# Optimization experiments

Hardware: AMD Instinct MI355X
Metric: run time of the kernel (lower is better)

Reference implementation:

```python
import jax, jax.numpy as jnp
import numpy as np

ENCODER_DIM = 2048
DECODER_DIM = 512
ATTENTION_DIM = 512
BATCH = 512
NUM_PIXELS = 196


def setup_inputs() -> dict:
    key = jax.random.key(0)
    k = jax.random.split(key, 8)
    s_e = 1.0 / np.sqrt(ENCODER_DIM)
    s_d = 1.0 / np.sqrt(DECODER_DIM)
    s_a = 1.0 / np.sqrt(ATTENTION_DIM)
    return {
        "encoder_out": jax.random.normal(k[0], (BATCH, NUM_PIXELS, ENCODER_DIM), jnp.float32),
        "decoder_hidden": jax.random.normal(k[1], (BATCH, DECODER_DIM), jnp.float32),
        "W_enc": jax.random.uniform(k[2], (ENCODER_DIM, ATTENTION_DIM), jnp.float32, -s_e, s_e),
        "b_enc": jax.random.uniform(k[3], (ATTENTION_DIM,), jnp.float32, -s_e, s_e),
        "W_dec": jax.random.uniform(k[4], (DECODER_DIM, ATTENTION_DIM), jnp.float32, -s_d, s_d),
        "b_dec": jax.random.uniform(k[5], (ATTENTION_DIM,), jnp.float32, -s_d, s_d),
        "W_full": jax.random.uniform(k[6], (ATTENTION_DIM,), jnp.float32, -s_a, s_a),
        "b_full": jax.random.uniform(k[7], (), jnp.float32, -s_a, s_a),
    }


def reference(encoder_out, decoder_hidden, W_enc, b_enc, W_dec, b_dec, W_full, b_full):
    # att1: [B, P, A], att2: [B, A]
    att1 = jnp.einsum('bpe,ea->bpa', encoder_out, W_enc) + b_enc
    att2 = decoder_hidden @ W_dec + b_dec
    # scores: [B, P]
    scores = jnp.einsum('bpa,a->bp', jnp.tanh(att1 + att2[:, None, :]), W_full) + b_full
    alpha = jax.nn.softmax(scores, axis=1)
    context = jnp.einsum('bpe,bp->be', encoder_out, alpha)
    return context, alpha
```

## Files before the change

### kernel.cpp

```cpp
#include <hip/hip_runtime.h>
#include <hip/hip_bf16.h>
#include <stdint.h>

#define BATCH 512
#define PIX   196
#define EDIM  2048
#define DDIM  512
#define ADIM  512
#define MROWS (BATCH*PIX)

#define BM 256
#define BN 256
#define BK 32
#define NT (EDIM/BK)

typedef __attribute__((ext_vector_type(8))) short bf16x8;
typedef __attribute__((ext_vector_type(8))) float f32x8;
typedef __attribute__((ext_vector_type(8))) __bf16 bf16v8;
typedef __attribute__((ext_vector_type(4))) float f32x4;

#define GLL16(g, lptr) __builtin_amdgcn_global_load_lds( \
    (const __attribute__((address_space(1))) void*)(g),  \
    (__attribute__((address_space(3))) void*)(lptr), 16, 0, 0)

static __device__ __forceinline__ unsigned short f2bf(float f) {
  union { float f; uint32_t u; } v; v.f = f;
  uint32_t u = v.u;
  return (unsigned short)((u + 0x7FFFu + ((u >> 16) & 1u)) >> 16);
}

static __device__ __forceinline__ bf16x8 cvt8(float4 a, float4 b) {
  f32x8 v = {a.x, a.y, a.z, a.w, b.x, b.y, b.z, b.w};
  bf16v8 c = __builtin_convertvector(v, bf16v8);
  bf16x8 r;
  __builtin_memcpy(&r, &c, 16);
  return r;
}

__global__ void k_transpose_wenc(const float* __restrict__ W,
                                 unsigned short* __restrict__ Bt) {
  __shared__ float tile[32][33];
  const int kt = blockIdx.x;
  const int nt = blockIdx.y;
  const int tx = threadIdx.x, ty = threadIdx.y;
#pragma unroll
  for (int j = 0; j < 4; j++)
    tile[ty + 8*j][tx] = W[(size_t)(kt*32 + ty + 8*j)*ADIM + nt*32 + tx];
  __syncthreads();
#pragma unroll
  for (int j = 0; j < 4; j++)
    Bt[(size_t)(nt*32 + ty + 8*j)*EDIM + kt*32 + tx] = f2bf(tile[tx][ty + 8*j]);
}

__global__ void k_att2(const float* __restrict__ H, const float* __restrict__ Wd,
                       const float* __restrict__ bd, float* __restrict__ att2) {
  __shared__ float h[DDIM];
  const int b = blockIdx.x;
  const int t = threadIdx.x;
  h[t]       = H[(size_t)b*DDIM + t];
  h[t + 256] = H[(size_t)b*DDIM + t + 256];
  __syncthreads();
  float a0 = 0.f, a1 = 0.f;
#pragma unroll 8
  for (int k = 0; k < DDIM; k++) {
    const float hv = h[k];
    a0 += hv * Wd[(size_t)k*ADIM + t];
    a1 += hv * Wd[(size_t)k*ADIM + t + 256];
  }
  att2[(size_t)b*ADIM + t]       = a0 + bd[t];
  att2[(size_t)b*ADIM + t + 256] = a1 + bd[t + 256];
}

__global__ __launch_bounds__(512) void k_gemm_scores(
    const float* __restrict__ enc,
    const unsigned short* __restrict__ Bt,
    const float* __restrict__ b_enc,
    const float* __restrict__ att2,
    const float* __restrict__ W_full,
    float* __restrict__ scores)
{
  __shared__ __align__(16) char ldsbuf[3*49152];
  __shared__ float sc[BM];
  char* ldsA = ldsbuf;
  char* ldsB = ldsbuf + 98304;

  const int t   = threadIdx.x;
  const int l   = t & 63;
  const int wid = t >> 6;
  const int wr  = wid >> 2;
  const int wc  = wid & 3;

  const int orig = blockIdx.x;
  const int tile = (orig & 7) * 98 + (orig >> 3);
  const int bm0 = (tile >> 1) * BM;
  const int bn0 = (tile & 1) * BN;

  if (t < BM) sc[t] = 0.f;

  const float* srcA[4];
#pragma unroll
  for (int j = 0; j < 4; j++) {
    const int idx = j*512 + t;
    const int row = idx >> 3, c = idx & 7;
    srcA[j] = enc + (size_t)(bm0 + row) * EDIM + (c ^ (row & 7)) * 4;
  }
  const unsigned short* srcB[2];
#pragma unroll
  for (int j = 0; j < 2; j++) {
    const int idx = j*512 + t;
    const int row = idx >> 2, c = idx & 3;
    srcB[j] = Bt + (size_t)(bn0 + row) * EDIM + (c ^ (row & 3)) * 8;
  }
  const int dstb = wid * 1024;

  const int l15 = l & 15, hi = l >> 4;
  const int sw7 = l15 & 7, sw3 = l15 & 3;
  const int addrA0 = (wr*128 + l15)*128 + (((2*hi)    ) ^ sw7)*16;
  const int addrA1 = (wr*128 + l15)*128 + (((2*hi) + 1) ^ sw7)*16;
  const int addrB  = (wc*64  + l15)*64  + (hi ^ sw3)*16;

  bf16x8 af[4], bfr[4];
  f32x4 acc[8][4] = {};

#define A_GLL(WB, KT) do {                                       \
    _Pragma("unroll")                                            \
    for (int j = 0; j < 4; j++)                                  \
      GLL16(srcA[j] + (size_t)(KT)*BK,                           \
            ldsA + (WB)*32768 + j*8192 + dstb);                  \
  } while (0)

#define B_GLL(WB, KT) do {                                       \
    _Pragma("unroll")                                            \
    for (int j = 0; j < 2; j++)                                  \
      GLL16(srcB[j] + (size_t)(KT)*BK,                           \
            ldsB + (WB)*16384 + j*8192 + dstb);                  \
  } while (0)

#define DSREAD_A(BUF, MOFF) do {                                 \
    _Pragma("unroll")                                            \
    for (int mi = 0; mi < 4; mi++) {                             \
      const float4 fa = *(const float4*)(ldsA + (BUF)*32768 + (mi+(MOFF))*2048 + addrA0); \
      const float4 fb = *(const float4*)(ldsA + (BUF)*32768 + (mi+(MOFF))*2048 + addrA1); \
      af[mi] = cvt8(fa, fb);                                     \
    }                                                            \
  } while (0)

#define DSREAD_B(BUF) do {                                       \
    _Pragma("unroll")                                            \
    for (int ni = 0; ni < 4; ni++)                               \
      bfr[ni] = *(const bf16x8*)(ldsB + (BUF)*16384 + ni*1024 + addrB); \
  } while (0)

#define BARLG()                                                  \
    __builtin_amdgcn_s_barrier();                                \
    asm volatile("s_waitcnt lgkmcnt(0)" ::: "memory");           \
    __builtin_amdgcn_sched_barrier(0);                           \
    __builtin_amdgcn_s_setprio(1)

#define ENDBAR()                                                 \
    __builtin_amdgcn_s_setprio(0);                               \
    __builtin_amdgcn_s_barrier()

#define MF16(MOFF) do {                                          \
    _Pragma("unroll")                                            \
    for (int mi = 0; mi < 4; mi++)                               \
      _Pragma("unroll")                                          \
      for (int ni = 0; ni < 4; ni++)                             \
        acc[mi+(MOFF)][ni] = __builtin_amdgcn_mfma_f32_16x16x32_bf16( \
            af[mi], bfr[ni], acc[mi+(MOFF)][ni], 0, 0, 0);       \
  } while (0)

#define TILE(T, BUF, WBUF, DO_STAGE, WVM) do {                   \
                                                         \
    if (DO_STAGE) A_GLL(WBUF, (T)+2);                            \
    DSREAD_B(BUF); DSREAD_A(BUF, 0);                             \
    BARLG(); MF16(0); ENDBAR();                                  \
                                                         \
    if (DO_STAGE) B_GLL(WBUF, (T)+2);                            \
    DSREAD_A(BUF, 4);                                            \
    BARLG(); MF16(4);                                            \
    if ((WVM) == 6)      asm volatile("s_waitcnt vmcnt(6)" ::: "memory"); \
    else if ((WVM) == 0) asm volatile("s_waitcnt vmcnt(0)" ::: "memory"); \
    ENDBAR();                                                    \
  } while (0)

  A_GLL(0, 0); B_GLL(0, 0);
  A_GLL(1, 1); B_GLL(1, 1);
  asm volatile("s_waitcnt vmcnt(6)" ::: "memory");
  __builtin_amdgcn_s_barrier();

  for (int kb = 0; kb < 60; kb += 3) {
    TILE(kb,     0, 2, true, 6);
    TILE(kb + 1, 1, 0, true, 6);
    TILE(kb + 2, 2, 1, true, 6);
  }
  TILE(60, 0, 2, true, 6);
  TILE(61, 1, 0, true, 6);
  TILE(62, 2, 2, false, 0);
  DSREAD_B(0); DSREAD_A(0, 0); MF16(0);
  DSREAD_A(0, 4); MF16(4);

  float be[4], wf[4];
  int colv[4];
#pragma unroll
  for (int ni = 0; ni < 4; ni++) {
    colv[ni] = bn0 + wc*64 + ni*16 + l15;
    be[ni] = b_enc[colv[ni]];
    wf[ni] = W_full[colv[ni]];
  }
#pragma unroll
  for (int mi = 0; mi < 8; mi++) {
#pragma unroll
    for (int e = 0; e < 4; e++) {
      const int row_l = wr*128 + mi*16 + hi*4 + e;
      const unsigned gr = (unsigned)(bm0 + row_l);
      const unsigned b  = gr / 196u;
      float s = 0.f;
#pragma unroll
      for (int ni = 0; ni < 4; ni++) {
        const float v = acc[mi][ni][e] + be[ni] + att2[(size_t)b*ADIM + colv[ni]];
        s += tanhf(v) * wf[ni];
      }
      s += __shfl_xor(s, 1); s += __shfl_xor(s, 2);
      s += __shfl_xor(s, 4); s += __shfl_xor(s, 8);
      if (l15 == 0) atomicAdd(&sc[row_l], s);
    }
  }
  __syncthreads();
  if (t < BM) atomicAdd(&scores[bm0 + t], sc[t]);
}

__global__ void k_softmax(float* __restrict__ sa) {
  __shared__ float red[256];
  const int b = blockIdx.x, t = threadIdx.x;
  const float v = (t < PIX) ? sa[(size_t)b*PIX + t] : -1e30f;
  red[t] = v; __syncthreads();
  for (int s2 = 128; s2 > 0; s2 >>= 1) {
    if (t < s2) red[t] = fmaxf(red[t], red[t + s2]);
    __syncthreads();
  }
  const float m = red[0]; __syncthreads();
  const float e = (t < PIX) ? __expf(v - m) : 0.f;
  red[t] = e; __syncthreads();
  for (int s2 = 128; s2 > 0; s2 >>= 1) {
    if (t < s2) red[t] += red[t + s2];
    __syncthreads();
  }
  const float inv = 1.f / red[0];
  if (t < PIX) sa[(size_t)b*PIX + t] = e * inv;
}

__global__ __launch_bounds__(512) void k_context(
    const float* __restrict__ enc, const float* __restrict__ alpha,
    float* __restrict__ ctx) {
  __shared__ float al[PIX];
  const int b = blockIdx.x, t = threadIdx.x;
  if (t < PIX) al[t] = alpha[(size_t)b*PIX + t];
  __syncthreads();
  const float4* e4 = (const float4*)(enc + (size_t)b * PIX * EDIM);
  float4 acc = {0.f, 0.f, 0.f, 0.f};
#pragma unroll 4
  for (int p = 0; p < PIX; p++) {
    const float4 v = e4[(size_t)p * (EDIM/4) + t];
    const float a = al[p];
    acc.x += v.x * a; acc.y += v.y * a; acc.z += v.z * a; acc.w += v.w * a;
  }
  ((float4*)(ctx + (size_t)b * EDIM))[t] = acc;
}

extern "C" void kernel_launch(void* const* d_in, const int* in_sizes, int n_in,
                              void* d_out, int out_size, void* d_ws, size_t ws_size,
                              hipStream_t stream) {
  (void)in_sizes; (void)n_in; (void)out_size; (void)ws_size;
  const float* enc   = (const float*)d_in[0];
  const float* hid   = (const float*)d_in[1];
  const float* Wenc  = (const float*)d_in[2];
  const float* benc  = (const float*)d_in[3];
  const float* Wdec  = (const float*)d_in[4];
  const float* bdec  = (const float*)d_in[5];
  const float* Wfull = (const float*)d_in[6];

  unsigned short* Bt = (unsigned short*)d_ws;
  float* att2 = (float*)((char*)d_ws + (size_t)ADIM * EDIM * 2);
  float* ctx   = (float*)d_out;
  float* alpha = (float*)d_out + (size_t)BATCH * EDIM;

  hipMemsetAsync(alpha, 0, (size_t)MROWS * sizeof(float), stream);
  k_transpose_wenc<<<dim3(64, 16), dim3(32, 8), 0, stream>>>(Wenc, Bt);
  k_att2<<<BATCH, 256, 0, stream>>>(hid, Wdec, bdec, att2);
  k_gemm_scores<<<784, 512, 0, stream>>>(enc, Bt, benc, att2, Wfull, alpha);
  k_softmax<<<BATCH, 256, 0, stream>>>(alpha);
  k_context<<<BATCH, 512, 0, stream>>>(enc, alpha, ctx);
}
```

Before: 667.3 us.

## Shrink GEMM tile to 256x128, convert A to bf16 in registers before LDS store

The fused score GEMM now uses 256-thread blocks with a 256x128 output tile and two blocks per CU, launching twice as many blocks. The A operand is loaded from global into registers, converted to bf16 once, and written to LDS in bf16. Previously it was staged as fp32 via global_load_lds and converted on every LDS read. LDS use drops sharply and the pipeline goes from three buffers to two, with a register-prefetched A tile. The trade-off is that the encoder tile is reread four times across N-tiles instead of twice, raising global traffic on the dominant fp32 input.

```diff
diff --git a/kernel.cpp b/kernel.cpp
--- a/kernel.cpp
+++ b/kernel.cpp
@@ -10,7 +10,7 @@
 #define MROWS (BATCH*PIX)
 
 #define BM 256
-#define BN 256
+#define BN 128
 #define BK 32
 #define NT (EDIM/BK)
 
@@ -71,7 +71,7 @@
   att2[(size_t)b*ADIM + t + 256] = a1 + bd[t + 256];
 }
 
-__global__ __launch_bounds__(512) void k_gemm_scores(
+__global__ __launch_bounds__(256, 2) void k_gemm_scores(
     const float* __restrict__ enc,
     const unsigned short* __restrict__ Bt,
     const float* __restrict__ b_enc,
@@ -79,87 +79,76 @@
     const float* __restrict__ W_full,
     float* __restrict__ scores)
 {
-  __shared__ __align__(16) char ldsbuf[3*49152];
+  __shared__ __align__(16) char ldsA[2*16384];
+  __shared__ __align__(16) char ldsB[2*8192];
   __shared__ float sc[BM];
-  char* ldsA = ldsbuf;
-  char* ldsB = ldsbuf + 98304;
 
   const int t   = threadIdx.x;
   const int l   = t & 63;
   const int wid = t >> 6;
-  const int wr  = wid >> 2;
-  const int wc  = wid & 3;
+  const int wr  = wid >> 1;
+  const int wc  = wid & 1;
 
   const int orig = blockIdx.x;
-  const int tile = (orig & 7) * 98 + (orig >> 3);
-  const int bm0 = (tile >> 1) * BM;
-  const int bn0 = (tile & 1) * BN;
-
-  if (t < BM) sc[t] = 0.f;
-
-  const float* srcA[4];
-#pragma unroll
-  for (int j = 0; j < 4; j++) {
-    const int idx = j*512 + t;
-    const int row = idx >> 3, c = idx & 7;
-    srcA[j] = enc + (size_t)(bm0 + row) * EDIM + (c ^ (row & 7)) * 4;
-  }
-  const unsigned short* srcB[2];
-#pragma unroll
-  for (int j = 0; j < 2; j++) {
-    const int idx = j*512 + t;
-    const int row = idx >> 2, c = idx & 3;
-    srcB[j] = Bt + (size_t)(bn0 + row) * EDIM + (c ^ (row & 3)) * 8;
-  }
-  const int dstb = wid * 1024;
+  const int tile = (orig & 7) * 196 + (orig >> 3);
+  const int bm0 = (tile >> 2) * BM;
+  const int bn0 = (tile & 3) * BN;
+
+  sc[t] = 0.f;
+
+  const int arow = t >> 2;
+  const int ap   = t & 3;
+  const float* srcA = enc + (size_t)(bm0 + arow) * EDIM + ap * 8;
+  const int wAb = arow*64 + ((ap ^ ((t >> 3) & 3)) * 16);
+
+  const unsigned short* srcB = Bt + (size_t)(bn0 + (t >> 2)) * EDIM
+                               + ((t & 3) ^ ((t >> 3) & 3)) * 8;
+  const int dB = wid * 1024;
 
   const int l15 = l & 15, hi = l >> 4;
-  const int sw7 = l15 & 7, sw3 = l15 & 3;
-  const int addrA0 = (wr*128 + l15)*128 + (((2*hi)    ) ^ sw7)*16;
-  const int addrA1 = (wr*128 + l15)*128 + (((2*hi) + 1) ^ sw7)*16;
-  const int addrB  = (wc*64  + l15)*64  + (hi ^ sw3)*16;
-
+  const int swl = (l15 >> 1) & 3;
+  const int addrA = (wr*128 + l15)*64 + ((hi ^ swl) * 16);
+  const int addrB = (wc*64  + l15)*64 + ((hi ^ swl) * 16);
+
+  float4 ar[2][4][2];
   bf16x8 af[4], bfr[4];
   f32x4 acc[8][4] = {};
 
-#define A_GLL(WB, KT) do {                                       \
-    _Pragma("unroll")                                            \
-    for (int j = 0; j < 4; j++)                                  \
-      GLL16(srcA[j] + (size_t)(KT)*BK,                           \
-            ldsA + (WB)*32768 + j*8192 + dstb);                  \
-  } while (0)
-
-#define B_GLL(WB, KT) do {                                       \
+#define A_ISSUE(SLOT, KT) do {                                   \
+    _Pragma("unroll")                                            \
+    for (int j = 0; j < 4; j++) {                                \
+      const float* _s = srcA + (size_t)(j)*64*EDIM + (KT)*BK;    \
+      ar[SLOT][j][0] = *(const float4*)(_s);                     \
+      ar[SLOT][j][1] = *(const float4*)(_s + 4);                 \
+    }                                                            \
+  } while (0)
+
+#define B_GLL(BUFI, KT) do {                                     \
     _Pragma("unroll")                                            \
     for (int j = 0; j < 2; j++)                                  \
-      GLL16(srcB[j] + (size_t)(KT)*BK,                           \
-            ldsB + (WB)*16384 + j*8192 + dstb);                  \
-  } while (0)
-
-#define DSREAD_A(BUF, MOFF) do {                                 \
-    _Pragma("unroll")                                            \
-    for (int mi = 0; mi < 4; mi++) {                             \
-      const float4 fa = *(const float4*)(ldsA + (BUF)*32768 + (mi+(MOFF))*2048 + addrA0); \
-      const float4 fb = *(const float4*)(ldsA + (BUF)*32768 + (mi+(MOFF))*2048 + addrA1); \
-      af[mi] = cvt8(fa, fb);                                     \
+      GLL16(srcB + (size_t)(j)*64*EDIM + (KT)*BK,                \
+            ldsB + (BUFI)*8192 + j*4096 + dB);                   \
+  } while (0)
+
+#define A_WRITE(BUFI, SLOT) do {                                 \
+    _Pragma("unroll")                                            \
+    for (int j = 0; j < 4; j++) {                                \
+      bf16x8 w = cvt8(ar[SLOT][j][0], ar[SLOT][j][1]);           \
+      *(bf16x8*)(ldsA + (BUFI)*16384 + wAb + j*4096) = w;        \
     }                                                            \
   } while (0)
 
-#define DSREAD_B(BUF) do {                                       \
+#define DSREAD_B(BUFI) do {                                      \
     _Pragma("unroll")                                            \
     for (int ni = 0; ni < 4; ni++)                               \
-      bfr[ni] = *(const bf16x8*)(ldsB + (BUF)*16384 + ni*1024 + addrB); \
-  } while (0)
-
-#define BARLG()                                                  \
-    __builtin_amdgcn_s_barrier();                                \
-    asm volatile("s_waitcnt lgkmcnt(0)" ::: "memory");           \
-    __builtin_amdgcn_sched_barrier(0);                           \
-    __builtin_amdgcn_s_setprio(1)
-
-#define ENDBAR()                                                 \
-    __builtin_amdgcn_s_setprio(0);                               \
-    __builtin_amdgcn_s_barrier()
+      bfr[ni] = *(const bf16x8*)(ldsB + (BUFI)*8192 + ni*1024 + addrB); \
+  } while (0)
+
+#define DSREAD_A(BUFI, MOFF) do {                                \
+    _Pragma("unroll")                                            \
+    for (int mi = 0; mi < 4; mi++)                               \
+      af[mi] = *(const bf16x8*)(ldsA + (BUFI)*16384 + (mi+(MOFF))*1024 + addrA); \
+  } while (0)
 
 #define MF16(MOFF) do {                                          \
     _Pragma("unroll")                                            \
@@ -170,35 +159,58 @@
             af[mi], bfr[ni], acc[mi+(MOFF)][ni], 0, 0, 0);       \
   } while (0)
 
-#define TILE(T, BUF, WBUF, DO_STAGE, WVM) do {                   \
-                                                         \
-    if (DO_STAGE) A_GLL(WBUF, (T)+2);                            \
-    DSREAD_B(BUF); DSREAD_A(BUF, 0);                             \
-    BARLG(); MF16(0); ENDBAR();                                  \
-                                                         \
-    if (DO_STAGE) B_GLL(WBUF, (T)+2);                            \
-    DSREAD_A(BUF, 4);                                            \
-    BARLG(); MF16(4);                                            \
-    if ((WVM) == 6)      asm volatile("s_waitcnt vmcnt(6)" ::: "memory"); \
-    else if ((WVM) == 0) asm volatile("s_waitcnt vmcnt(0)" ::: "memory"); \
-    ENDBAR();                                                    \
-  } while (0)
-
-  A_GLL(0, 0); B_GLL(0, 0);
-  A_GLL(1, 1); B_GLL(1, 1);
-  asm volatile("s_waitcnt vmcnt(6)" ::: "memory");
+#define LGKM0_SB()                                               \
+    asm volatile("s_waitcnt lgkmcnt(0)" ::: "memory");           \
+    __builtin_amdgcn_sched_barrier(0)
+
+#define TILE_STEADY(T, CUR, NXT) do {                            \
+    B_GLL(NXT, (T)+1);                                           \
+    A_ISSUE(CUR, (T)+2);                                         \
+    DSREAD_B(CUR); DSREAD_A(CUR, 0);                             \
+    LGKM0_SB();                                                  \
+    __builtin_amdgcn_s_setprio(1); MF16(0); __builtin_amdgcn_s_setprio(0); \
+    DSREAD_A(CUR, 4);                                            \
+    LGKM0_SB();                                                  \
+    __builtin_amdgcn_s_setprio(1); MF16(4); __builtin_amdgcn_s_setprio(0); \
+    asm volatile("s_waitcnt vmcnt(10)" ::: "memory");            \
+    A_WRITE(NXT, NXT);                                           \
+    asm volatile("s_waitcnt vmcnt(8) lgkmcnt(0)" ::: "memory");  \
+    __builtin_amdgcn_s_barrier();                                \
+  } while (0)
+
+  A_ISSUE(0, 0);
+  B_GLL(0, 0);
+  A_ISSUE(1, 1);
+  asm volatile("s_waitcnt vmcnt(10)" ::: "memory");
+  A_WRITE(0, 0);
+  asm volatile("s_waitcnt vmcnt(8) lgkmcnt(0)" ::: "memory");
   __builtin_amdgcn_s_barrier();
 
-  for (int kb = 0; kb < 60; kb += 3) {
-    TILE(kb,     0, 2, true, 6);
-    TILE(kb + 1, 1, 0, true, 6);
-    TILE(kb + 2, 2, 1, true, 6);
-  }
-  TILE(60, 0, 2, true, 6);
-  TILE(61, 1, 0, true, 6);
-  TILE(62, 2, 2, false, 0);
-  DSREAD_B(0); DSREAD_A(0, 0); MF16(0);
-  DSREAD_A(0, 4); MF16(4);
+  for (int kb = 0; kb < 62; kb += 2) {
+    TILE_STEADY(kb,     0, 1);
+    TILE_STEADY(kb + 1, 1, 0);
+  }
+  {
+    B_GLL(1, 63);
+    DSREAD_B(0); DSREAD_A(0, 0);
+    LGKM0_SB();
+    __builtin_amdgcn_s_setprio(1); MF16(0); __builtin_amdgcn_s_setprio(0);
+    DSREAD_A(0, 4);
+    LGKM0_SB();
+    __builtin_amdgcn_s_setprio(1); MF16(4); __builtin_amdgcn_s_setprio(0);
+    asm volatile("s_waitcnt vmcnt(2)" ::: "memory");
+    A_WRITE(1, 1);
+    asm volatile("s_waitcnt vmcnt(0) lgkmcnt(0)" ::: "memory");
+    __builtin_amdgcn_s_barrier();
+  }
+  {
+    DSREAD_B(1); DSREAD_A(1, 0);
+    LGKM0_SB();
+    MF16(0);
+    DSREAD_A(1, 4);
+    LGKM0_SB();
+    MF16(4);
+  }
 
   float be[4], wf[4];
   int colv[4];
@@ -227,7 +239,7 @@
     }
   }
   __syncthreads();
-  if (t < BM) atomicAdd(&scores[bm0 + t], sc[t]);
+  atomicAdd(&scores[bm0 + t], sc[t]);
 }
 
 __global__ void k_softmax(float* __restrict__ sa) {
@@ -288,7 +300,7 @@
   hipMemsetAsync(alpha, 0, (size_t)MROWS * sizeof(float), stream);
   k_transpose_wenc<<<dim3(64, 16), dim3(32, 8), 0, stream>>>(Wenc, Bt);
   k_att2<<<BATCH, 256, 0, stream>>>(hid, Wdec, bdec, att2);
-  k_gemm_scores<<<784, 512, 0, stream>>>(enc, Bt, benc, att2, Wfull, alpha);
+  k_gemm_scores<<<1568, 256, 0, stream>>>(enc, Bt, benc, att2, Wfull, alpha);
   k_softmax<<<BATCH, 256, 0, stream>>>(alpha);
   k_context<<<BATCH, 512, 0, stream>>>(enc, alpha, ctx);
 }
```

Result: no change. 671.3 us (+0.6%).
